# Kernel tuning notes

Measured on AMD Instinct MI355X. Metric: run time of the kernel, lower is better.

## Reference

```python
import jax, jax.numpy as jnp
import numpy as np

B, N, D, K = 16, 16384, 256, 32
EPS = 1e-12  # torch F.normalize eps


def setup_inputs() -> dict:
    key = jax.random.key(0)
    k1, k2, k3, k4 = jax.random.split(key, 4)
    stddev = 1.0 / np.sqrt(D)
    x = jax.random.normal(k1, (B, N, D), dtype=jnp.float32)
    W = jax.random.normal(k2, (K, D), dtype=jnp.float32) * stddev  # fc weight
    b = jax.random.normal(k3, (K,), dtype=jnp.float32) * stddev    # fc bias
    k_mean = jax.random.normal(k4, (K, D), dtype=jnp.float32) * stddev
    return {"x": x, "W": W, "b": b, "k_mean": k_mean}


def reference(x, W, b, k_mean):
    # soft assignment: (B, N, K)
    logits = jnp.einsum("bnd,kd->bnk", x, W) + b
    a = jax.nn.softmax(logits, axis=2)
    # VLAD aggregation, fused form of sum_n a[b,n,k] * (x[b,n,:] - k_mean[k,:]):
    #   v[b,k,:] = sum_n a[b,n,k] x[b,n,:]  -  (sum_n a[b,n,k]) * k_mean[k,:]
    a_sum = jnp.sum(a, axis=1)                       # (B, K)
    v = jnp.einsum("bnk,bnd->bkd", a, x) - a_sum[..., None] * k_mean[None]
    # intra-normalize over d
    v = v / jnp.maximum(jnp.linalg.norm(v, axis=2, keepdims=True), EPS)
    # flatten and L2-normalize
    v = v.reshape(v.shape[0], -1)                    # (B, K*D)
    v = v / jnp.maximum(jnp.linalg.norm(v, axis=1, keepdims=True), EPS)
    return v
```

## Files before the change

kernel.cpp:

```cpp
#include <hip/hip_runtime.h>
#include <hip/hip_bf16.h>
#include <math.h>

#define BB 16
#define NN 16384
#define DD 256
#define KK 32

typedef short bf16x8 __attribute__((ext_vector_type(8)));
typedef float f32x4 __attribute__((ext_vector_type(4)));

__device__ inline unsigned pk2(float lo, float hi) {
    __hip_bfloat162 h = __float22bfloat162_rn(make_float2(lo, hi));
    union { __hip_bfloat162 h; unsigned u; } v; v.h = h;
    return v.u;
}
__device__ inline bf16x8 u4bf(uint4 q) {
    union { uint4 u; bf16x8 v; } c; c.u = q; return c.v;
}

#define CAE(vv, e) ((e) == 0 ? (vv).x : (e) == 1 ? (vv).y : (e) == 2 ? (vv).z : (vv).w)

__launch_bounds__(256, 1)
__global__ void netvlad_k1(const float* __restrict__ x,
                           const float* __restrict__ W,
                           const float* __restrict__ bias,
                           float* __restrict__ vpart,
                           float* __restrict__ apart) {
    __shared__ __align__(16) char lds[49152];

    const int t   = threadIdx.x;
    const int l   = t & 63;
    const int w   = t >> 6;
    const int l15 = l & 15;
    const int lg4 = l >> 4;
    const int bid = blockIdx.x;
    const int b   = bid >> 4;
    const int blk = bid & 15;

    for (int i = 0; i < 8; i++) {
        int f = i * 256 + t;
        int k = f >> 6, c4 = f & 63;
        float4 wv = ((const float4*)W)[f];
        int byte = k * 512 + ((c4 * 8) ^ ((k & 7) << 4));
        *(uint2*)(lds + byte) = make_uint2(pk2(wv.x, wv.y), pk2(wv.z, wv.w));
    }
    const float cb0 = bias[l15];
    const float cb1 = bias[16 + l15];
    __syncthreads();

    char* xtw = lds + 16384 + w * 8192;

    f32x4 acc0[16], acc1[16];
#pragma unroll
    for (int i = 0; i < 16; i++) { acc0[i] = (f32x4){0,0,0,0}; acc1[i] = (f32x4){0,0,0,0}; }
    float asr0 = 0.f, asr1 = 0.f;

    const float* xbase = x + ((size_t)b * NN + (size_t)blk * 1024) * DD;

    float4 pf[16];
    {
        const float* xr = xbase + (size_t)(w * 16 + l15) * DD + lg4 * 8;
#pragma unroll
        for (int ks = 0; ks < 8; ks++) {
            pf[2 * ks]     = *(const float4*)(xr + ks * 32);
            pf[2 * ks + 1] = *(const float4*)(xr + ks * 32 + 4);
        }
    }

    uint4 af0 = make_uint4(0, 0, 0, 0), af1 = make_uint4(0, 0, 0, 0);

#pragma unroll 1
    for (int s = 0; s < 16; s++) {
        const float* xsub = xbase + ((size_t)s * 64 + (size_t)w * 16) * DD;

        float4 ca[8];
#pragma unroll
        for (int i = 0; i < 8; i++)
            ca[i] = *(const float4*)(xsub + (size_t)i * DD + l * 4);

        if (s > 0) {
#pragma unroll
            for (int dt = 0; dt < 16; dt++) {
                int d = dt * 16 + l15;
                unsigned sw = ((unsigned)(d >> 3) & 1u) << 4;
                uint2 bl = *(const uint2*)(xtw + d * 32 + ((lg4 * 8) ^ sw));
                bf16x8 bv = u4bf(make_uint4(bl.x, bl.y, 0, 0));
                acc0[dt] = __builtin_amdgcn_mfma_f32_16x16x32_bf16(u4bf(af0), bv, acc0[dt], 0, 0, 0);
                acc1[dt] = __builtin_amdgcn_mfma_f32_16x16x32_bf16(u4bf(af1), bv, acc1[dt], 0, 0, 0);
            }
        }

#pragma unroll
        for (int half = 0; half < 2; half++) {
            if (half == 1) {
#pragma unroll
                for (int i = 0; i < 8; i++)
                    ca[i] = *(const float4*)(xsub + (size_t)(8 + i) * DD + l * 4);
            }
#pragma unroll
            for (int e = 0; e < 4; e++) {
                int d = 4 * l + e;
                unsigned sw = ((unsigned)(d >> 3) & 1u) << 4;
                uint4 q;
                q.x = pk2(CAE(ca[0], e), CAE(ca[1], e));
                q.y = pk2(CAE(ca[2], e), CAE(ca[3], e));
                q.z = pk2(CAE(ca[4], e), CAE(ca[5], e));
                q.w = pk2(CAE(ca[6], e), CAE(ca[7], e));
                *(uint4*)(xtw + d * 32 + (((unsigned)(half * 16)) ^ sw)) = q;
            }
        }

        f32x4 c0 = (f32x4){cb0, cb0, cb0, cb0};
        f32x4 c1 = (f32x4){cb1, cb1, cb1, cb1};
        {
            const unsigned swk = ((unsigned)(l15 & 7)) << 4;
#pragma unroll
            for (int ks = 0; ks < 8; ks++) {
                uint4 xq;
                xq.x = pk2(pf[2 * ks].x,     pf[2 * ks].y);
                xq.y = pk2(pf[2 * ks].z,     pf[2 * ks].w);
                xq.z = pk2(pf[2 * ks + 1].x, pf[2 * ks + 1].y);
                xq.w = pk2(pf[2 * ks + 1].z, pf[2 * ks + 1].w);
                bf16x8 ax = u4bf(xq);
                bf16x8 w0 = *(const bf16x8*)(lds + l15 * 512        + (((unsigned)(ks * 64 + lg4 * 16)) ^ swk));
                bf16x8 w1 = *(const bf16x8*)(lds + (16 + l15) * 512 + (((unsigned)(ks * 64 + lg4 * 16)) ^ swk));
                c0 = __builtin_amdgcn_mfma_f32_16x16x32_bf16(ax, w0, c0, 0, 0, 0);
                c1 = __builtin_amdgcn_mfma_f32_16x16x32_bf16(ax, w1, c1, 0, 0, 0);
            }
        }

        if (s < 15) {
            const float* xr = xbase + ((size_t)(s + 1) * 64 + (size_t)(w * 16 + l15)) * DD + lg4 * 8;
#pragma unroll
            for (int ks = 0; ks < 8; ks++) {
                pf[2 * ks]     = *(const float4*)(xr + ks * 32);
                pf[2 * ks + 1] = *(const float4*)(xr + ks * 32 + 4);
            }
        }

        float a0v[4], a1v[4];
#pragma unroll
        for (int r = 0; r < 4; r++) {
            float m = fmaxf(c0[r], c1[r]);
            m = fmaxf(m, __shfl_xor(m, 1));
            m = fmaxf(m, __shfl_xor(m, 2));
            m = fmaxf(m, __shfl_xor(m, 4));
            m = fmaxf(m, __shfl_xor(m, 8));
            float p0 = __expf(c0[r] - m), p1 = __expf(c1[r] - m);
            float ss = p0 + p1;
            ss += __shfl_xor(ss, 1);
            ss += __shfl_xor(ss, 2);
            ss += __shfl_xor(ss, 4);
            ss += __shfl_xor(ss, 8);
            float inv = 1.0f / ss;
            a0v[r] = p0 * inv; a1v[r] = p1 * inv;
        }
        asr0 += a0v[0] + a0v[1] + a0v[2] + a0v[3];
        asr1 += a1v[0] + a1v[1] + a1v[2] + a1v[3];
        af0 = make_uint4(pk2(a0v[0], a0v[1]), pk2(a0v[2], a0v[3]), 0, 0);
        af1 = make_uint4(pk2(a1v[0], a1v[1]), pk2(a1v[2], a1v[3]), 0, 0);
    }

#pragma unroll
    for (int dt = 0; dt < 16; dt++) {
        int d = dt * 16 + l15;
        unsigned sw = ((unsigned)(d >> 3) & 1u) << 4;
        uint2 bl = *(const uint2*)(xtw + d * 32 + ((lg4 * 8) ^ sw));
        bf16x8 bv = u4bf(make_uint4(bl.x, bl.y, 0, 0));
        acc0[dt] = __builtin_amdgcn_mfma_f32_16x16x32_bf16(u4bf(af0), bv, acc0[dt], 0, 0, 0);
        acc1[dt] = __builtin_amdgcn_mfma_f32_16x16x32_bf16(u4bf(af1), bv, acc1[dt], 0, 0, 0);
    }

    asr0 += __shfl_xor(asr0, 16);  asr0 += __shfl_xor(asr0, 32);
    asr1 += __shfl_xor(asr1, 16);  asr1 += __shfl_xor(asr1, 32);
    if (l < 16) {
        float* ap = apart + ((size_t)bid * 4 + w) * KK;
        ap[l15]      = asr0;
        ap[16 + l15] = asr1;
    }

    __syncthreads();
    float* vb = (float*)lds;
    if ((w & 1) == 0) {
    }
    if (w == 0) {
#pragma unroll
        for (int dt = 0; dt < 16; dt++) {
            int d = dt * 16 + l15;
#pragma unroll
            for (int r = 0; r < 4; r++) {
                int k0 = lg4 * 4 + r;
                vb[k0 * 260 + d]        = acc0[dt][r];
                vb[(16 + k0) * 260 + d] = acc1[dt][r];
            }
        }
    }
    __syncthreads();
    if (w == 1 || w == 2) {
        if (w == 1) {
#pragma unroll
            for (int dt = 0; dt < 16; dt++) {
                int d = dt * 16 + l15;
#pragma unroll
                for (int r = 0; r < 4; r++) {
                    int k0 = lg4 * 4 + r;
                    vb[k0 * 260 + d]        += acc0[dt][r];
                    vb[(16 + k0) * 260 + d] += acc1[dt][r];
                }
            }
        }
    }
    __syncthreads();
    if (w == 2) {
#pragma unroll
        for (int dt = 0; dt < 16; dt++) {
            int d = dt * 16 + l15;
#pragma unroll
            for (int r = 0; r < 4; r++) {
                int k0 = lg4 * 4 + r;
                vb[k0 * 260 + d]        += acc0[dt][r];
                vb[(16 + k0) * 260 + d] += acc1[dt][r];
            }
        }
    }
    __syncthreads();
    if (w == 3) {
#pragma unroll
        for (int dt = 0; dt < 16; dt++) {
            int d = dt * 16 + l15;
#pragma unroll
            for (int r = 0; r < 4; r++) {
                int k0 = lg4 * 4 + r;
                vb[k0 * 260 + d]        += acc0[dt][r];
                vb[(16 + k0) * 260 + d] += acc1[dt][r];
            }
        }
    }
    __syncthreads();
    float* vp = vpart + (size_t)bid * KK * DD;
#pragma unroll
    for (int i = 0; i < 8; i++) {
        int f = i * 256 + t;
        int k = f >> 6, c4 = f & 63;
        f32x4 v4 = *(const f32x4*)&vb[k * 260 + c4 * 4];
        *(f32x4*)&vp[(size_t)k * DD + c4 * 4] = v4;
    }
}

__global__ void netvlad_kC(const float* __restrict__ vpart,
                           const float* __restrict__ apart,
                           const float* __restrict__ kmean,
                           float* __restrict__ out) {
    const int bi = blockIdx.x / KK;
    const int k  = blockIdx.x % KK;
    const int t  = threadIdx.x;

    float v = 0.0f;
    for (int j = 0; j < 16; j++)
        v += vpart[(((size_t)bi * 16 + j) * KK + k) * DD + t];

    float asum = 0.0f;
    for (int j = 0; j < 64; j++)
        asum += apart[((size_t)bi * 64 + j) * KK + k];

    v -= asum * kmean[(size_t)k * DD + t];

    float sq = v * v;
    sq += __shfl_xor(sq, 1);  sq += __shfl_xor(sq, 2);  sq += __shfl_xor(sq, 4);
    sq += __shfl_xor(sq, 8);  sq += __shfl_xor(sq, 16); sq += __shfl_xor(sq, 32);
    __shared__ float red[4];
    if ((t & 63) == 0) red[t >> 6] = sq;
    __syncthreads();
    float tot = red[0] + red[1] + red[2] + red[3];

    const float EPS = 1e-12f;
    float invn = 1.0f / fmaxf(sqrtf(tot), EPS);
    const float invK = 0.1767766952966369f;
    out[((size_t)bi * KK + k) * DD + t] = v * invn * invK;
}

extern "C" void kernel_launch(void* const* d_in, const int* in_sizes, int n_in,
                              void* d_out, int out_size, void* d_ws, size_t ws_size,
                              hipStream_t stream) {
    const float* x     = (const float*)d_in[0];
    const float* W     = (const float*)d_in[1];
    const float* bias  = (const float*)d_in[2];
    const float* kmean = (const float*)d_in[3];
    float* out = (float*)d_out;

    float* vpart = (float*)d_ws;
    float* apart = vpart + (size_t)256 * KK * DD;

    hipLaunchKernelGGL(netvlad_k1, dim3(256), dim3(256), 0, stream,
                       x, W, bias, vpart, apart);
    hipLaunchKernelGGL(netvlad_kC, dim3(BB * KK), dim3(256), 0, stream,
                       vpart, apart, kmean, out);
}
```

Measured before the change: 67.86 us.

## Reuse logits-stage bf16 x tile via LDS for aggregation instead of reloading from global

Instead of reloading each 64-row x sub-tile from global memory a second time for the VLAD aggregation transpose, the bf16-packed x fragments already converted for the logit MFMA are stored to a swizzled LDS buffer. The next iteration transposes them into the aggregation layout. This makes the aggregation lag two steps behind the softmax, with an extra drain step after the loop. It halves global reads of x and removes a duplicate fp32-to-bf16 conversion, at the cost of 32 KB more LDS and extra LDS traffic.

```diff
diff --git a/kernel.cpp b/kernel.cpp
--- a/kernel.cpp
+++ b/kernel.cpp
@@ -19,7 +19,7 @@
     union { uint4 u; bf16x8 v; } c; c.u = q; return c.v;
 }
 
-#define CAE(vv, e) ((e) == 0 ? (vv).x : (e) == 1 ? (vv).y : (e) == 2 ? (vv).z : (vv).w)
+#define UE(v, e) ((e) == 0 ? (v).x : (e) == 1 ? (v).y : (e) == 2 ? (v).z : (v).w)
 
 __launch_bounds__(256, 1)
 __global__ void netvlad_k1(const float* __restrict__ x,
@@ -27,7 +27,7 @@
                            const float* __restrict__ bias,
                            float* __restrict__ vpart,
                            float* __restrict__ apart) {
-    __shared__ __align__(16) char lds[49152];
+    __shared__ __align__(16) char lds[81920];
 
     const int t   = threadIdx.x;
     const int l   = t & 63;
@@ -49,7 +49,8 @@
     const float cb1 = bias[16 + l15];
     __syncthreads();
 
-    char* xtw = lds + 16384 + w * 8192;
+    char* xhw = lds + 16384 + w * 8192;
+    char* xtw = lds + 49152 + w * 8192;
 
     f32x4 acc0[16], acc1[16];
 #pragma unroll
@@ -68,66 +69,72 @@
         }
     }
 
-    uint4 af0 = make_uint4(0, 0, 0, 0), af1 = make_uint4(0, 0, 0, 0);
+    uint4 af0_m1 = make_uint4(0,0,0,0), af1_m1 = make_uint4(0,0,0,0);
+    uint4 af0_m2 = make_uint4(0,0,0,0), af1_m2 = make_uint4(0,0,0,0);
 
 #pragma unroll 1
     for (int s = 0; s < 16; s++) {
-        const float* xsub = xbase + ((size_t)s * 64 + (size_t)w * 16) * DD;
-
-        float4 ca[8];
-#pragma unroll
-        for (int i = 0; i < 8; i++)
-            ca[i] = *(const float4*)(xsub + (size_t)i * DD + l * 4);
-
-        if (s > 0) {
+        if (s > 1) {
 #pragma unroll
             for (int dt = 0; dt < 16; dt++) {
                 int d = dt * 16 + l15;
                 unsigned sw = ((unsigned)(d >> 3) & 1u) << 4;
                 uint2 bl = *(const uint2*)(xtw + d * 32 + ((lg4 * 8) ^ sw));
                 bf16x8 bv = u4bf(make_uint4(bl.x, bl.y, 0, 0));
-                acc0[dt] = __builtin_amdgcn_mfma_f32_16x16x32_bf16(u4bf(af0), bv, acc0[dt], 0, 0, 0);
-                acc1[dt] = __builtin_amdgcn_mfma_f32_16x16x32_bf16(u4bf(af1), bv, acc1[dt], 0, 0, 0);
-            }
-        }
-
-#pragma unroll
-        for (int half = 0; half < 2; half++) {
-            if (half == 1) {
-#pragma unroll
-                for (int i = 0; i < 8; i++)
-                    ca[i] = *(const float4*)(xsub + (size_t)(8 + i) * DD + l * 4);
-            }
-#pragma unroll
-            for (int e = 0; e < 4; e++) {
-                int d = 4 * l + e;
-                unsigned sw = ((unsigned)(d >> 3) & 1u) << 4;
-                uint4 q;
-                q.x = pk2(CAE(ca[0], e), CAE(ca[1], e));
-                q.y = pk2(CAE(ca[2], e), CAE(ca[3], e));
-                q.z = pk2(CAE(ca[4], e), CAE(ca[5], e));
-                q.w = pk2(CAE(ca[6], e), CAE(ca[7], e));
-                *(uint4*)(xtw + d * 32 + (((unsigned)(half * 16)) ^ sw)) = q;
+                acc0[dt] = __builtin_amdgcn_mfma_f32_16x16x32_bf16(u4bf(af0_m2), bv, acc0[dt], 0, 0, 0);
+                acc1[dt] = __builtin_amdgcn_mfma_f32_16x16x32_bf16(u4bf(af1_m2), bv, acc1[dt], 0, 0, 0);
+            }
+        }
+
+        if (s > 0) {
+#pragma unroll
+            for (int half = 0; half < 2; half++) {
+                ushort4 cv[8];
+#pragma unroll
+                for (int i = 0; i < 8; i++) {
+                    int r  = half * 8 + i;
+                    int us = r * 256 + ((((4 * l) & ~7) ^ ((r & 7) << 3)) | ((4 * l) & 7));
+                    cv[i] = *(const ushort4*)(xhw + us * 2);
+                }
+#pragma unroll
+                for (int e = 0; e < 4; e++) {
+                    uint4 q;
+                    q.x = (unsigned)UE(cv[0], e) | ((unsigned)UE(cv[1], e) << 16);
+                    q.y = (unsigned)UE(cv[2], e) | ((unsigned)UE(cv[3], e) << 16);
+                    q.z = (unsigned)UE(cv[4], e) | ((unsigned)UE(cv[5], e) << 16);
+                    q.w = (unsigned)UE(cv[6], e) | ((unsigned)UE(cv[7], e) << 16);
+                    int d = 4 * l + e;
+                    unsigned sw = ((unsigned)(d >> 3) & 1u) << 4;
+                    *(uint4*)(xtw + d * 32 + (((unsigned)(half * 16)) ^ sw)) = q;
+                }
             }
         }
 
         f32x4 c0 = (f32x4){cb0, cb0, cb0, cb0};
         f32x4 c1 = (f32x4){cb1, cb1, cb1, cb1};
+        uint4 xq[8];
         {
             const unsigned swk = ((unsigned)(l15 & 7)) << 4;
 #pragma unroll
             for (int ks = 0; ks < 8; ks++) {
-                uint4 xq;
-                xq.x = pk2(pf[2 * ks].x,     pf[2 * ks].y);
-                xq.y = pk2(pf[2 * ks].z,     pf[2 * ks].w);
-                xq.z = pk2(pf[2 * ks + 1].x, pf[2 * ks + 1].y);
-                xq.w = pk2(pf[2 * ks + 1].z, pf[2 * ks + 1].w);
-                bf16x8 ax = u4bf(xq);
+                uint4 q;
+                q.x = pk2(pf[2 * ks].x,     pf[2 * ks].y);
+                q.y = pk2(pf[2 * ks].z,     pf[2 * ks].w);
+                q.z = pk2(pf[2 * ks + 1].x, pf[2 * ks + 1].y);
+                q.w = pk2(pf[2 * ks + 1].z, pf[2 * ks + 1].w);
+                xq[ks] = q;
+                bf16x8 ax = u4bf(q);
                 bf16x8 w0 = *(const bf16x8*)(lds + l15 * 512        + (((unsigned)(ks * 64 + lg4 * 16)) ^ swk));
                 bf16x8 w1 = *(const bf16x8*)(lds + (16 + l15) * 512 + (((unsigned)(ks * 64 + lg4 * 16)) ^ swk));
                 c0 = __builtin_amdgcn_mfma_f32_16x16x32_bf16(ax, w0, c0, 0, 0, 0);
                 c1 = __builtin_amdgcn_mfma_f32_16x16x32_bf16(ax, w1, c1, 0, 0, 0);
             }
+        }
+
+#pragma unroll
+        for (int ks = 0; ks < 8; ks++) {
+            int us = l15 * 256 + ((ks * 32 + lg4 * 8) ^ ((l15 & 7) << 3));
+            *(uint4*)(xhw + us * 2) = xq[ks];
         }
 
         if (s < 15) {
@@ -158,8 +165,9 @@
         }
         asr0 += a0v[0] + a0v[1] + a0v[2] + a0v[3];
         asr1 += a1v[0] + a1v[1] + a1v[2] + a1v[3];
-        af0 = make_uint4(pk2(a0v[0], a0v[1]), pk2(a0v[2], a0v[3]), 0, 0);
-        af1 = make_uint4(pk2(a1v[0], a1v[1]), pk2(a1v[2], a1v[3]), 0, 0);
+        af0_m2 = af0_m1;  af1_m2 = af1_m1;
+        af0_m1 = make_uint4(pk2(a0v[0], a0v[1]), pk2(a0v[2], a0v[3]), 0, 0);
+        af1_m1 = make_uint4(pk2(a1v[0], a1v[1]), pk2(a1v[2], a1v[3]), 0, 0);
     }
 
 #pragma unroll
@@ -168,8 +176,38 @@
         unsigned sw = ((unsigned)(d >> 3) & 1u) << 4;
         uint2 bl = *(const uint2*)(xtw + d * 32 + ((lg4 * 8) ^ sw));
         bf16x8 bv = u4bf(make_uint4(bl.x, bl.y, 0, 0));
-        acc0[dt] = __builtin_amdgcn_mfma_f32_16x16x32_bf16(u4bf(af0), bv, acc0[dt], 0, 0, 0);
-        acc1[dt] = __builtin_amdgcn_mfma_f32_16x16x32_bf16(u4bf(af1), bv, acc1[dt], 0, 0, 0);
+        acc0[dt] = __builtin_amdgcn_mfma_f32_16x16x32_bf16(u4bf(af0_m2), bv, acc0[dt], 0, 0, 0);
+        acc1[dt] = __builtin_amdgcn_mfma_f32_16x16x32_bf16(u4bf(af1_m2), bv, acc1[dt], 0, 0, 0);
+    }
+#pragma unroll
+    for (int half = 0; half < 2; half++) {
+        ushort4 cv[8];
+#pragma unroll
+        for (int i = 0; i < 8; i++) {
+            int r  = half * 8 + i;
+            int us = r * 256 + ((((4 * l) & ~7) ^ ((r & 7) << 3)) | ((4 * l) & 7));
+            cv[i] = *(const ushort4*)(xhw + us * 2);
+        }
+#pragma unroll
+        for (int e = 0; e < 4; e++) {
+            uint4 q;
+            q.x = (unsigned)UE(cv[0], e) | ((unsigned)UE(cv[1], e) << 16);
+            q.y = (unsigned)UE(cv[2], e) | ((unsigned)UE(cv[3], e) << 16);
+            q.z = (unsigned)UE(cv[4], e) | ((unsigned)UE(cv[5], e) << 16);
+            q.w = (unsigned)UE(cv[6], e) | ((unsigned)UE(cv[7], e) << 16);
+            int d = 4 * l + e;
+            unsigned sw = ((unsigned)(d >> 3) & 1u) << 4;
+            *(uint4*)(xtw + d * 32 + (((unsigned)(half * 16)) ^ sw)) = q;
+        }
+    }
+#pragma unroll
+    for (int dt = 0; dt < 16; dt++) {
+        int d = dt * 16 + l15;
+        unsigned sw = ((unsigned)(d >> 3) & 1u) << 4;
+        uint2 bl = *(const uint2*)(xtw + d * 32 + ((lg4 * 8) ^ sw));
+        bf16x8 bv = u4bf(make_uint4(bl.x, bl.y, 0, 0));
+        acc0[dt] = __builtin_amdgcn_mfma_f32_16x16x32_bf16(u4bf(af0_m1), bv, acc0[dt], 0, 0, 0);
+        acc1[dt] = __builtin_amdgcn_mfma_f32_16x16x32_bf16(u4bf(af1_m1), bv, acc1[dt], 0, 0, 0);
     }
 
     asr0 += __shfl_xor(asr0, 16);  asr0 += __shfl_xor(asr0, 32);
@@ -182,8 +220,6 @@
 
     __syncthreads();
     float* vb = (float*)lds;
-    if ((w & 1) == 0) {
-    }
     if (w == 0) {
 #pragma unroll
         for (int dt = 0; dt < 16; dt++) {
@@ -197,17 +233,15 @@
         }
     }
     __syncthreads();
-    if (w == 1 || w == 2) {
-        if (w == 1) {
-#pragma unroll
-            for (int dt = 0; dt < 16; dt++) {
-                int d = dt * 16 + l15;
-#pragma unroll
-                for (int r = 0; r < 4; r++) {
-                    int k0 = lg4 * 4 + r;
-                    vb[k0 * 260 + d]        += acc0[dt][r];
-                    vb[(16 + k0) * 260 + d] += acc1[dt][r];
-                }
+    if (w == 1) {
+#pragma unroll
+        for (int dt = 0; dt < 16; dt++) {
+            int d = dt * 16 + l15;
+#pragma unroll
+            for (int r = 0; r < 4; r++) {
+                int k0 = lg4 * 4 + r;
+                vb[k0 * 260 + d]        += acc0[dt][r];
+                vb[(16 + k0) * 260 + d] += acc1[dt][r];
             }
         }
     }
```

After: 60.06 us. -11.5%, faster.
